# Performance work log

Measured on AMD Instinct MI355X. Metric: run time of the kernel, lower is better.

Reference implementation:

```python
import jax, jax.numpy as jnp
import numpy as np

B, NF, L, K = 128, 64, 4096, 64  # batch, num_filters, winlen, latent_dim
NG = 400  # gaussians per filter
SIGMA = 16.0  # fixed Filter_xp sigma


def setup_inputs() -> dict:
    key = jax.random.key(0)
    ks = jax.random.split(key, 14)
    w = lambda k, shp: (jax.random.normal(k, shp, jnp.float32) * 0.05)
    return {
        "X": jax.random.normal(ks[0], (B, NG, L), jnp.float32),
        "eps": jax.random.normal(ks[1], (B, K), jnp.float32),
        "mus": jax.random.uniform(ks[2], (NF, NG), jnp.float32, 0.0, float(L)),
        "amps": jax.random.uniform(ks[3], (NF, NG), jnp.float32),
        "Wmu": w(ks[4], (K, NF)), "bmu": w(ks[5], (K,)),
        "Wsig": w(ks[6], (K, NF)), "bsig": w(ks[7], (K,)),
        "W01": w(ks[8], (K, K)), "b01": w(ks[9], (K,)),
        "W1": w(ks[10], (NG, K)), "b1": w(ks[11], (NG,)),
        "W2": w(ks[12], (NG, K)), "b2": w(ks[13], (NG,)),
        "winlen": L,
    }


def reference(X, eps, mus, amps, Wmu, bmu, Wsig, bsig, W01, b01, W1, b1, W2, b2, winlen):
    # Batched Gaussian filter bank: (NF, NG, L); torch.linspace(0, winlen, winlen)
    x = jnp.linspace(0.0, float(winlen), winlen)
    filt = jnp.exp(-(x[None, None, :] - mus[:, :, None]) ** 2 / (2.0 * SIGMA ** 2)) * amps[:, :, None]
    # All filters' 'bij,ij->b' reductions in one pass -> (B, NF)
    filtered = jnp.einsum('bij,fij->bf', X, filt) / winlen
    mu = jax.nn.elu(filtered @ Wmu.T + bmu)
    log_sig = jax.nn.elu(filtered @ Wsig.T + bsig)
    latent = mu + eps * jnp.exp(log_sig)  # reparameterize
    h = jax.nn.gelu(latent @ W01.T + b01, approximate=False)
    coms = jax.nn.gelu(h @ W1.T + b1, approximate=False)
    pred_num_spikes = jax.nn.gelu(h @ W2.T + b2, approximate=False)
    return (coms, pred_num_spikes, mu, log_sig)
```

## Files before the change

kernel.cpp:

```cpp
#include <hip/hip_runtime.h>
#include <cstdint>
#include <cstddef>

#define B_   128
#define NF_  64
#define L_   4096
#define K_   64
#define NG_  400

#define GP_     8
#define GITER_  (NG_ / GP_)
#define ROWS_   2
#define PADF_   128
#define ROWPF_  (PADF_ + L_ + PADF_)

constexpr float STEP = 4096.0f / 4095.0f;
constexpr float NEGC = -1.4426950408889634f / 512.0f;

__global__ __launch_bounds__(512, 4) void filt_kernel(
    const float* __restrict__ X, const float* __restrict__ mus,
    const float* __restrict__ amps, float* __restrict__ part)
{
    const int p  = blockIdx.x;
    const int b0 = blockIdx.y * ROWS_;
    const int t  = threadIdx.x;
    const int f  = t >> 3;
    const int i  = t & 7;

    __shared__ __align__(16) float Xs[2][ROWS_][ROWPF_];

    if (t < 256) {
        const int br = t >> 6;
        const int k  = t & 63;
        float4* pr = (float4*)Xs[br >> 1][br & 1];
        const float4 z{0.f, 0.f, 0.f, 0.f};
        if (k < 32) pr[k] = z;
        else        pr[1056 + (k - 32)] = z;
    }

    const float* __restrict__ Xb0 = X + ((size_t)(b0 + 0) * NG_) * L_;
    const float* __restrict__ Xb1 = X + ((size_t)(b0 + 1) * NG_) * L_;

    int g = p * GITER_;
    float4 xv[4];
    {
        const float4* r0 = (const float4*)(Xb0 + (size_t)g * L_);
        const float4* r1 = (const float4*)(Xb1 + (size_t)g * L_);
        xv[0] = r0[t]; xv[1] = r0[t + 512];
        xv[2] = r1[t]; xv[3] = r1[t + 512];
    }
    float mu_c = mus [f * NG_ + g];
    float sc_c = amps[f * NG_ + g] * (1.0f / 4096.0f);
    {
        float4* d0 = (float4*)(Xs[0][0] + PADF_);
        float4* d1 = (float4*)(Xs[0][1] + PADF_);
        d0[t] = xv[0]; d0[t + 512] = xv[1];
        d1[t] = xv[2]; d1[t + 512] = xv[3];
    }
    __syncthreads();

    float acc0 = 0.f, acc1 = 0.f;
    float mu_n = 0.f, sc_n = 0.f;

    for (int it = 0; it < GITER_; ++it) {
        const int  cur  = it & 1;
        const bool more = (it + 1 < GITER_);
        const int  gn   = g + 1;

        if (more) {
            const float4* r0 = (const float4*)(Xb0 + (size_t)gn * L_);
            const float4* r1 = (const float4*)(Xb1 + (size_t)gn * L_);
            xv[0] = r0[t]; xv[1] = r0[t + 512];
            xv[2] = r1[t]; xv[3] = r1[t + 512];
            mu_n = mus [f * NG_ + gn];
            sc_n = amps[f * NG_ + gn] * (1.0f / 4096.0f);
        }

        const int   l0 = (((int)mu_c) - 96) & ~3;
        const float bx = fmaf((float)(l0 + 4 * i), STEP, -mu_c);
        float w[6][4];
#pragma unroll
        for (int c = 0; c < 6; ++c)
#pragma unroll
            for (int j = 0; j < 4; ++j) {
                const float d = bx + (float)(32 * c + j) * STEP;
                w[c][j] = exp2f(NEGC * d * d);
            }

        const float* x0 = Xs[cur][0] + PADF_ + l0 + 4 * i;
        const float* x1 = Xs[cur][1] + PADF_ + l0 + 4 * i;
        float d0 = 0.f, d1 = 0.f;
#pragma unroll
        for (int c = 0; c < 6; ++c) {
            const float4 a = *(const float4*)(x0 + 32 * c);
            const float4 b = *(const float4*)(x1 + 32 * c);
            d0 = fmaf(a.x, w[c][0], fmaf(a.y, w[c][1], fmaf(a.z, w[c][2], fmaf(a.w, w[c][3], d0))));
            d1 = fmaf(b.x, w[c][0], fmaf(b.y, w[c][1], fmaf(b.z, w[c][2], fmaf(b.w, w[c][3], d1))));
        }
        acc0 = fmaf(sc_c, d0, acc0);
        acc1 = fmaf(sc_c, d1, acc1);

        if (more) {
            const int nxt = cur ^ 1;
            float4* e0 = (float4*)(Xs[nxt][0] + PADF_);
            float4* e1 = (float4*)(Xs[nxt][1] + PADF_);
            e0[t] = xv[0]; e0[t + 512] = xv[1];
            e1[t] = xv[2]; e1[t + 512] = xv[3];
            mu_c = mu_n; sc_c = sc_n; g = gn;
            __syncthreads();
        }
    }

#pragma unroll
    for (int d = 1; d < 8; d <<= 1) {
        acc0 += __shfl_xor(acc0, d);
        acc1 += __shfl_xor(acc1, d);
    }
    if (i == 0) {
        part[((size_t)p * B_ + b0    ) * NF_ + f] = acc0;
        part[((size_t)p * B_ + b0 + 1) * NF_ + f] = acc1;
    }
}

__device__ __forceinline__ float gelu_exact(float x) {
    return 0.5f * x * (1.0f + erff(x * 0.70710678118654752f));
}

__global__ __launch_bounds__(256) void head_kernel(
    const float* __restrict__ part, const float* __restrict__ eps,
    const float* __restrict__ Wmu,  const float* __restrict__ bmu,
    const float* __restrict__ Wsig, const float* __restrict__ bsig,
    const float* __restrict__ W01,  const float* __restrict__ b01,
    const float* __restrict__ W1,   const float* __restrict__ b1,
    const float* __restrict__ W2,   const float* __restrict__ b2,
    float* __restrict__ out)
{
    const int b = blockIdx.x;
    const int t = threadIdx.x;
    __shared__ float fil[NF_], lat[K_], hh[K_];

    if (t < NF_) {
        float s = 0.f;
#pragma unroll
        for (int pp = 0; pp < GP_; ++pp)
            s += part[((size_t)pp * B_ + b) * NF_ + t];
        fil[t] = s;
    }
    __syncthreads();

    if (t < K_) {
        float am = bmu[t], as = bsig[t];
#pragma unroll 8
        for (int fj = 0; fj < NF_; ++fj) {
            float x = fil[fj];
            am = fmaf(x, Wmu [t * NF_ + fj], am);
            as = fmaf(x, Wsig[t * NF_ + fj], as);
        }
        float muv = am > 0.0f ? am : expm1f(am);
        float lsv = as > 0.0f ? as : expm1f(as);
        out[2 * B_ * NG_            + b * K_ + t] = muv;
        out[2 * B_ * NG_ + B_ * K_  + b * K_ + t] = lsv;
        lat[t] = fmaf(eps[b * K_ + t], expf(lsv), muv);
    }
    __syncthreads();

    if (t < K_) {
        float a = b01[t];
#pragma unroll 8
        for (int j = 0; j < K_; ++j) a = fmaf(lat[j], W01[t * K_ + j], a);
        hh[t] = gelu_exact(a);
    }
    __syncthreads();

    for (int n = t; n < NG_; n += 256) {
        float a1 = b1[n], a2 = b2[n];
#pragma unroll 8
        for (int k = 0; k < K_; ++k) {
            float hk = hh[k];
            a1 = fmaf(hk, W1[n * K_ + k], a1);
            a2 = fmaf(hk, W2[n * K_ + k], a2);
        }
        out[            b * NG_ + n] = gelu_exact(a1);
        out[B_ * NG_ +  b * NG_ + n] = gelu_exact(a2);
    }
}

extern "C" void kernel_launch(void* const* d_in, const int* in_sizes, int n_in,
                              void* d_out, int out_size, void* d_ws, size_t ws_size,
                              hipStream_t stream) {
    const float* X    = (const float*)d_in[0];
    const float* eps  = (const float*)d_in[1];
    const float* mus  = (const float*)d_in[2];
    const float* amps = (const float*)d_in[3];
    const float* Wmu  = (const float*)d_in[4];
    const float* bmu  = (const float*)d_in[5];
    const float* Wsig = (const float*)d_in[6];
    const float* bsig = (const float*)d_in[7];
    const float* W01  = (const float*)d_in[8];
    const float* b01  = (const float*)d_in[9];
    const float* W1   = (const float*)d_in[10];
    const float* b1   = (const float*)d_in[11];
    const float* W2   = (const float*)d_in[12];
    const float* b2   = (const float*)d_in[13];

    float* out  = (float*)d_out;
    float* part = (float*)d_ws;

    filt_kernel<<<dim3(GP_, B_ / ROWS_), 512, 0, stream>>>(X, mus, amps, part);
    head_kernel<<<B_, 256, 0, stream>>>(part, eps, Wmu, bmu, Wsig, bsig,
                                        W01, b01, W1, b1, W2, b2, out);
}
```

Baseline: 166.9 us.

## Deepen X prefetch to two tiles, use lighter barriers, split head kernel across output chunks

The filter kernel now keeps two register sets of X rows in flight, loading tile it+2 while computing tile it. The loop is unrolled by two so the register buffers alternate statically. The block barrier is replaced with an LDS-only waitcnt plus s_barrier, so outstanding global loads no longer stall at each sync. The head kernel gets a grid dimension of 4, each block computing 100 of the 400 outputs; the small shared prefix is recomputed in every block. The deeper prefetch raises register pressure under launch_bounds(512,4).

```diff
diff --git a/kernel.cpp b/kernel.cpp
--- a/kernel.cpp
+++ b/kernel.cpp
@@ -25,7 +25,7 @@
     const int b0 = blockIdx.y * ROWS_;
     const int t  = threadIdx.x;
     const int f  = t >> 3;
-    const int i  = t & 7;
+    const int i8 = t & 7;
 
     __shared__ __align__(16) float Xs[2][ROWS_][ROWPF_];
 
@@ -40,75 +40,72 @@
 
     const float* __restrict__ Xb0 = X + ((size_t)(b0 + 0) * NG_) * L_;
     const float* __restrict__ Xb1 = X + ((size_t)(b0 + 1) * NG_) * L_;
-
-    int g = p * GITER_;
-    float4 xv[4];
-    {
-        const float4* r0 = (const float4*)(Xb0 + (size_t)g * L_);
-        const float4* r1 = (const float4*)(Xb1 + (size_t)g * L_);
-        xv[0] = r0[t]; xv[1] = r0[t + 512];
-        xv[2] = r1[t]; xv[3] = r1[t + 512];
-    }
-    float mu_c = mus [f * NG_ + g];
-    float sc_c = amps[f * NG_ + g] * (1.0f / 4096.0f);
-    {
-        float4* d0 = (float4*)(Xs[0][0] + PADF_);
-        float4* d1 = (float4*)(Xs[0][1] + PADF_);
-        d0[t] = xv[0]; d0[t + 512] = xv[1];
-        d1[t] = xv[2]; d1[t + 512] = xv[3];
-    }
-    __syncthreads();
+    const int gs = p * GITER_;
+
+    float4 xvA[4], xvB[4];
+
+#define LOADT(xv, g) {                                                   \
+        const float4* r0 = (const float4*)(Xb0 + (size_t)(g) * L_);      \
+        const float4* r1 = (const float4*)(Xb1 + (size_t)(g) * L_);      \
+        xv[0] = r0[t]; xv[1] = r0[t + 512];                              \
+        xv[2] = r1[t]; xv[3] = r1[t + 512]; }
+
+#define WRITET(xv, buf) {                                                \
+        float4* e0 = (float4*)(Xs[buf][0] + PADF_);                      \
+        float4* e1 = (float4*)(Xs[buf][1] + PADF_);                      \
+        e0[t] = xv[0]; e0[t + 512] = xv[1];                              \
+        e1[t] = xv[2]; e1[t + 512] = xv[3]; }
+
+#define BARRIER() {                                                      \
+        asm volatile("s_waitcnt lgkmcnt(0)" ::: "memory");               \
+        __builtin_amdgcn_s_barrier();                                    \
+        __builtin_amdgcn_sched_barrier(0); }
+
+    LOADT(xvA, gs + 0);
+    float mu_c = mus [f * NG_ + gs];
+    float sc_c = amps[f * NG_ + gs] * (1.0f / 4096.0f);
+    LOADT(xvB, gs + 1);
+    WRITET(xvA, 0);
+    BARRIER();
 
     float acc0 = 0.f, acc1 = 0.f;
-    float mu_n = 0.f, sc_n = 0.f;
-
-    for (int it = 0; it < GITER_; ++it) {
-        const int  cur  = it & 1;
-        const bool more = (it + 1 < GITER_);
-        const int  gn   = g + 1;
-
-        if (more) {
-            const float4* r0 = (const float4*)(Xb0 + (size_t)gn * L_);
-            const float4* r1 = (const float4*)(Xb1 + (size_t)gn * L_);
-            xv[0] = r0[t]; xv[1] = r0[t + 512];
-            xv[2] = r1[t]; xv[3] = r1[t + 512];
-            mu_n = mus [f * NG_ + gn];
-            sc_n = amps[f * NG_ + gn] * (1.0f / 4096.0f);
-        }
-
-        const int   l0 = (((int)mu_c) - 96) & ~3;
-        const float bx = fmaf((float)(l0 + 4 * i), STEP, -mu_c);
-        float w[6][4];
-#pragma unroll
-        for (int c = 0; c < 6; ++c)
-#pragma unroll
-            for (int j = 0; j < 4; ++j) {
-                const float d = bx + (float)(32 * c + j) * STEP;
-                w[c][j] = exp2f(NEGC * d * d);
-            }
-
-        const float* x0 = Xs[cur][0] + PADF_ + l0 + 4 * i;
-        const float* x1 = Xs[cur][1] + PADF_ + l0 + 4 * i;
-        float d0 = 0.f, d1 = 0.f;
-#pragma unroll
-        for (int c = 0; c < 6; ++c) {
-            const float4 a = *(const float4*)(x0 + 32 * c);
-            const float4 b = *(const float4*)(x1 + 32 * c);
-            d0 = fmaf(a.x, w[c][0], fmaf(a.y, w[c][1], fmaf(a.z, w[c][2], fmaf(a.w, w[c][3], d0))));
-            d1 = fmaf(b.x, w[c][0], fmaf(b.y, w[c][1], fmaf(b.z, w[c][2], fmaf(b.w, w[c][3], d1))));
-        }
-        acc0 = fmaf(sc_c, d0, acc0);
-        acc1 = fmaf(sc_c, d1, acc1);
-
-        if (more) {
-            const int nxt = cur ^ 1;
-            float4* e0 = (float4*)(Xs[nxt][0] + PADF_);
-            float4* e1 = (float4*)(Xs[nxt][1] + PADF_);
-            e0[t] = xv[0]; e0[t + 512] = xv[1];
-            e1[t] = xv[2]; e1[t + 512] = xv[3];
-            mu_c = mu_n; sc_c = sc_n; g = gn;
-            __syncthreads();
-        }
+
+#define BODY(it, regsI, regsW) {                                         \
+        if ((it) + 2 < GITER_) LOADT(regsI, gs + (it) + 2);              \
+        const float mu = mu_c;                                           \
+        const float sc = sc_c;                                           \
+        {   const int gn = gs + (((it) + 1 < GITER_) ? (it) + 1 : (it)); \
+            mu_c = mus [f * NG_ + gn];                                   \
+            sc_c = amps[f * NG_ + gn] * (1.0f / 4096.0f); }              \
+        const int   l0 = (((int)mu) - 96) & ~3;                          \
+        const float bx = fmaf((float)(l0 + 4 * i8), STEP, -mu);          \
+        float wgt[6][4];                                                 \
+        _Pragma("unroll")                                                \
+        for (int c = 0; c < 6; ++c)                                      \
+            _Pragma("unroll")                                            \
+            for (int j = 0; j < 4; ++j) {                                \
+                const float d = bx + (float)(32 * c + j) * STEP;         \
+                wgt[c][j] = exp2f(NEGC * d * d);                         \
+            }                                                            \
+        const float* x0 = Xs[(it) & 1][0] + PADF_ + l0 + 4 * i8;         \
+        const float* x1 = Xs[(it) & 1][1] + PADF_ + l0 + 4 * i8;         \
+        float d0 = 0.f, d1 = 0.f;                                        \
+        _Pragma("unroll")                                                \
+        for (int c = 0; c < 6; ++c) {                                    \
+            const float4 a = *(const float4*)(x0 + 32 * c);              \
+            const float4 b = *(const float4*)(x1 + 32 * c);              \
+            d0 = fmaf(a.x, wgt[c][0], fmaf(a.y, wgt[c][1],               \
+                 fmaf(a.z, wgt[c][2], fmaf(a.w, wgt[c][3], d0))));       \
+            d1 = fmaf(b.x, wgt[c][0], fmaf(b.y, wgt[c][1],               \
+                 fmaf(b.z, wgt[c][2], fmaf(b.w, wgt[c][3], d1))));       \
+        }                                                                \
+        acc0 = fmaf(sc, d0, acc0);                                       \
+        acc1 = fmaf(sc, d1, acc1);                                       \
+        if ((it) + 1 < GITER_) { WRITET(regsW, ((it) + 1) & 1); BARRIER(); } }
+
+    for (int it = 0; it < GITER_; it += 2) {
+        BODY(it,     xvA, xvB);
+        BODY(it + 1, xvB, xvA);
     }
 
 #pragma unroll
@@ -116,10 +113,14 @@
         acc0 += __shfl_xor(acc0, d);
         acc1 += __shfl_xor(acc1, d);
     }
-    if (i == 0) {
+    if (i8 == 0) {
         part[((size_t)p * B_ + b0    ) * NF_ + f] = acc0;
         part[((size_t)p * B_ + b0 + 1) * NF_ + f] = acc1;
     }
+#undef LOADT
+#undef WRITET
+#undef BARRIER
+#undef BODY
 }
 
 __device__ __forceinline__ float gelu_exact(float x) {
@@ -136,6 +137,7 @@
     float* __restrict__ out)
 {
     const int b = blockIdx.x;
+    const int q = blockIdx.y;
     const int t = threadIdx.x;
     __shared__ float fil[NF_], lat[K_], hh[K_];
 
@@ -158,8 +160,10 @@
         }
         float muv = am > 0.0f ? am : expm1f(am);
         float lsv = as > 0.0f ? as : expm1f(as);
-        out[2 * B_ * NG_            + b * K_ + t] = muv;
-        out[2 * B_ * NG_ + B_ * K_  + b * K_ + t] = lsv;
+        if (q == 0) {
+            out[2 * B_ * NG_            + b * K_ + t] = muv;
+            out[2 * B_ * NG_ + B_ * K_  + b * K_ + t] = lsv;
+        }
         lat[t] = fmaf(eps[b * K_ + t], expf(lsv), muv);
     }
     __syncthreads();
@@ -172,7 +176,8 @@
     }
     __syncthreads();
 
-    for (int n = t; n < NG_; n += 256) {
+    const int n0 = q * 100, n1 = n0 + 100;
+    for (int n = n0 + t; n < n1; n += 256) {
         float a1 = b1[n], a2 = b2[n];
 #pragma unroll 8
         for (int k = 0; k < K_; ++k) {
@@ -207,6 +212,6 @@
     float* part = (float*)d_ws;
 
     filt_kernel<<<dim3(GP_, B_ / ROWS_), 512, 0, stream>>>(X, mus, amps, part);
-    head_kernel<<<B_, 256, 0, stream>>>(part, eps, Wmu, bmu, Wsig, bsig,
-                                        W01, b01, W1, b1, W2, b2, out);
-}
+    head_kernel<<<dim3(B_, 4), 256, 0, stream>>>(part, eps, Wmu, bmu, Wsig, bsig,
+                                                 W01, b01, W1, b1, W2, b2, out);
+}
```

New measurement: 365.0 us. 2.19x slower.

## Double filter-kernel block size to 16 lanes per filter and split head over outputs

Applied to the files above, without the earlier changes.

The filter kernel moves from 512 to 1024 threads per block, with 16 lanes per filter instead of 8. Each lane now computes 3 chunks of Gaussian weights instead of 6, and each thread loads one float4 per row per gaussian instead of two. The head kernel is split across 4 blocks per batch row, each producing 100 of the 400 outputs, to expose more parallelism. The price is that the small latent MLP is recomputed four times per batch row. The 1024-thread blocks with launch bounds of 8 also add register pressure.

```diff
diff --git a/kernel.cpp b/kernel.cpp
--- a/kernel.cpp
+++ b/kernel.cpp
@@ -17,15 +17,15 @@
 constexpr float STEP = 4096.0f / 4095.0f;
 constexpr float NEGC = -1.4426950408889634f / 512.0f;
 
-__global__ __launch_bounds__(512, 4) void filt_kernel(
+__global__ __launch_bounds__(1024, 8) void filt_kernel(
     const float* __restrict__ X, const float* __restrict__ mus,
     const float* __restrict__ amps, float* __restrict__ part)
 {
-    const int p  = blockIdx.x;
-    const int b0 = blockIdx.y * ROWS_;
-    const int t  = threadIdx.x;
-    const int f  = t >> 3;
-    const int i  = t & 7;
+    const int p   = blockIdx.x;
+    const int b0  = blockIdx.y * ROWS_;
+    const int t   = threadIdx.x;
+    const int f   = t >> 4;
+    const int i16 = t & 15;
 
     __shared__ __align__(16) float Xs[2][ROWS_][ROWPF_];
 
@@ -40,83 +40,68 @@
 
     const float* __restrict__ Xb0 = X + ((size_t)(b0 + 0) * NG_) * L_;
     const float* __restrict__ Xb1 = X + ((size_t)(b0 + 1) * NG_) * L_;
-
-    int g = p * GITER_;
-    float4 xv[4];
-    {
-        const float4* r0 = (const float4*)(Xb0 + (size_t)g * L_);
-        const float4* r1 = (const float4*)(Xb1 + (size_t)g * L_);
-        xv[0] = r0[t]; xv[1] = r0[t + 512];
-        xv[2] = r1[t]; xv[3] = r1[t + 512];
-    }
-    float mu_c = mus [f * NG_ + g];
-    float sc_c = amps[f * NG_ + g] * (1.0f / 4096.0f);
-    {
-        float4* d0 = (float4*)(Xs[0][0] + PADF_);
-        float4* d1 = (float4*)(Xs[0][1] + PADF_);
-        d0[t] = xv[0]; d0[t + 512] = xv[1];
-        d1[t] = xv[2]; d1[t + 512] = xv[3];
-    }
+    const int gs = p * GITER_;
+
+    float4 xv0 = ((const float4*)(Xb0 + (size_t)gs * L_))[t];
+    float4 xv1 = ((const float4*)(Xb1 + (size_t)gs * L_))[t];
+    float mu_c = mus [f * NG_ + gs];
+    float sc_c = amps[f * NG_ + gs] * (1.0f / 4096.0f);
+    ((float4*)(Xs[0][0] + PADF_))[t] = xv0;
+    ((float4*)(Xs[0][1] + PADF_))[t] = xv1;
     __syncthreads();
 
     float acc0 = 0.f, acc1 = 0.f;
-    float mu_n = 0.f, sc_n = 0.f;
 
     for (int it = 0; it < GITER_; ++it) {
         const int  cur  = it & 1;
         const bool more = (it + 1 < GITER_);
-        const int  gn   = g + 1;
+        const int  g    = gs + it;
 
         if (more) {
-            const float4* r0 = (const float4*)(Xb0 + (size_t)gn * L_);
-            const float4* r1 = (const float4*)(Xb1 + (size_t)gn * L_);
-            xv[0] = r0[t]; xv[1] = r0[t + 512];
-            xv[2] = r1[t]; xv[3] = r1[t + 512];
-            mu_n = mus [f * NG_ + gn];
-            sc_n = amps[f * NG_ + gn] * (1.0f / 4096.0f);
-        }
-
-        const int   l0 = (((int)mu_c) - 96) & ~3;
-        const float bx = fmaf((float)(l0 + 4 * i), STEP, -mu_c);
-        float w[6][4];
-#pragma unroll
-        for (int c = 0; c < 6; ++c)
+            xv0 = ((const float4*)(Xb0 + (size_t)(g + 1) * L_))[t];
+            xv1 = ((const float4*)(Xb1 + (size_t)(g + 1) * L_))[t];
+        }
+        const float mu = mu_c;
+        const float sc = sc_c;
+        if (more) {
+            mu_c = mus [f * NG_ + g + 1];
+            sc_c = amps[f * NG_ + g + 1] * (1.0f / 4096.0f);
+        }
+
+        const int   l0 = (((int)mu) - 96) & ~3;
+        const float bx = fmaf((float)(l0 + 4 * i16), STEP, -mu);
+        const float* x0 = Xs[cur][0] + PADF_ + l0 + 4 * i16;
+        const float* x1 = Xs[cur][1] + PADF_ + l0 + 4 * i16;
+        float d0 = 0.f, d1 = 0.f;
+#pragma unroll
+        for (int c = 0; c < 3; ++c) {
+            float w[4];
 #pragma unroll
             for (int j = 0; j < 4; ++j) {
-                const float d = bx + (float)(32 * c + j) * STEP;
-                w[c][j] = exp2f(NEGC * d * d);
+                const float d = bx + (float)(64 * c + j) * STEP;
+                w[j] = exp2f(NEGC * d * d);
             }
-
-        const float* x0 = Xs[cur][0] + PADF_ + l0 + 4 * i;
-        const float* x1 = Xs[cur][1] + PADF_ + l0 + 4 * i;
-        float d0 = 0.f, d1 = 0.f;
-#pragma unroll
-        for (int c = 0; c < 6; ++c) {
-            const float4 a = *(const float4*)(x0 + 32 * c);
-            const float4 b = *(const float4*)(x1 + 32 * c);
-            d0 = fmaf(a.x, w[c][0], fmaf(a.y, w[c][1], fmaf(a.z, w[c][2], fmaf(a.w, w[c][3], d0))));
-            d1 = fmaf(b.x, w[c][0], fmaf(b.y, w[c][1], fmaf(b.z, w[c][2], fmaf(b.w, w[c][3], d1))));
-        }
-        acc0 = fmaf(sc_c, d0, acc0);
-        acc1 = fmaf(sc_c, d1, acc1);
+            const float4 a = *(const float4*)(x0 + 64 * c);
+            const float4 b = *(const float4*)(x1 + 64 * c);
+            d0 = fmaf(a.x, w[0], fmaf(a.y, w[1], fmaf(a.z, w[2], fmaf(a.w, w[3], d0))));
+            d1 = fmaf(b.x, w[0], fmaf(b.y, w[1], fmaf(b.z, w[2], fmaf(b.w, w[3], d1))));
+        }
+        acc0 = fmaf(sc, d0, acc0);
+        acc1 = fmaf(sc, d1, acc1);
 
         if (more) {
-            const int nxt = cur ^ 1;
-            float4* e0 = (float4*)(Xs[nxt][0] + PADF_);
-            float4* e1 = (float4*)(Xs[nxt][1] + PADF_);
-            e0[t] = xv[0]; e0[t + 512] = xv[1];
-            e1[t] = xv[2]; e1[t + 512] = xv[3];
-            mu_c = mu_n; sc_c = sc_n; g = gn;
+            ((float4*)(Xs[cur ^ 1][0] + PADF_))[t] = xv0;
+            ((float4*)(Xs[cur ^ 1][1] + PADF_))[t] = xv1;
             __syncthreads();
         }
     }
 
 #pragma unroll
-    for (int d = 1; d < 8; d <<= 1) {
+    for (int d = 1; d < 16; d <<= 1) {
         acc0 += __shfl_xor(acc0, d);
         acc1 += __shfl_xor(acc1, d);
     }
-    if (i == 0) {
+    if (i16 == 0) {
         part[((size_t)p * B_ + b0    ) * NF_ + f] = acc0;
         part[((size_t)p * B_ + b0 + 1) * NF_ + f] = acc1;
     }
@@ -136,6 +121,7 @@
     float* __restrict__ out)
 {
     const int b = blockIdx.x;
+    const int q = blockIdx.y;
     const int t = threadIdx.x;
     __shared__ float fil[NF_], lat[K_], hh[K_];
 
@@ -158,8 +144,10 @@
         }
         float muv = am > 0.0f ? am : expm1f(am);
         float lsv = as > 0.0f ? as : expm1f(as);
-        out[2 * B_ * NG_            + b * K_ + t] = muv;
-        out[2 * B_ * NG_ + B_ * K_  + b * K_ + t] = lsv;
+        if (q == 0) {
+            out[2 * B_ * NG_            + b * K_ + t] = muv;
+            out[2 * B_ * NG_ + B_ * K_  + b * K_ + t] = lsv;
+        }
         lat[t] = fmaf(eps[b * K_ + t], expf(lsv), muv);
     }
     __syncthreads();
@@ -172,7 +160,8 @@
     }
     __syncthreads();
 
-    for (int n = t; n < NG_; n += 256) {
+    const int n0 = q * 100, n1 = n0 + 100;
+    for (int n = n0 + t; n < n1; n += 256) {
         float a1 = b1[n], a2 = b2[n];
 #pragma unroll 8
         for (int k = 0; k < K_; ++k) {
@@ -206,7 +195,7 @@
     float* out  = (float*)d_out;
     float* part = (float*)d_ws;
 
-    filt_kernel<<<dim3(GP_, B_ / ROWS_), 512, 0, stream>>>(X, mus, amps, part);
-    head_kernel<<<B_, 256, 0, stream>>>(part, eps, Wmu, bmu, Wsig, bsig,
-                                        W01, b01, W1, b1, W2, b2, out);
-}
+    filt_kernel<<<dim3(GP_, B_ / ROWS_), 1024, 0, stream>>>(X, mus, amps, part);
+    head_kernel<<<dim3(B_, 4), 256, 0, stream>>>(part, eps, Wmu, bmu, Wsig, bsig,
+                                                 W01, b01, W1, b1, W2, b2, out);
+}
```

After: 160.5 us. 1.04x faster.
